# Kernel tuning notes

Measured on AMD Instinct MI355X. Metric: run time of the kernel, lower is better.

The kernel has to match this reference:

```python
import jax, jax.numpy as jnp
import numpy as np

N_NODES = 100000
N_EDGES = 1600000
IN_FEATS = 128
HEADS = 4
OUT_FEATS = 16
NEG_SLOPE = 0.2  # DGL GATConv default negative_slope


def setup_inputs() -> dict:
    key = jax.random.key(0)
    ks = jax.random.split(key, 7)
    feats = jax.random.normal(ks[0], (N_NODES, IN_FEATS), dtype=jnp.float32)
    W = jax.random.normal(ks[1], (HEADS * OUT_FEATS, IN_FEATS), dtype=jnp.float32) * 0.05
    attn_l = jax.random.normal(ks[2], (HEADS, OUT_FEATS), dtype=jnp.float32) * 0.1
    attn_r = jax.random.normal(ks[3], (HEADS, OUT_FEATS), dtype=jnp.float32) * 0.1
    bias = jax.random.normal(ks[4], (HEADS * OUT_FEATS,), dtype=jnp.float32) * 0.01
    src = jax.random.randint(ks[5], (N_EDGES,), 0, N_NODES, dtype=jnp.int64 if jax.config.jax_enable_x64 else jnp.int32)
    dst = jax.random.randint(ks[6], (N_EDGES,), 0, N_NODES, dtype=jnp.int64 if jax.config.jax_enable_x64 else jnp.int32)
    return {"feats": feats, "W": W, "attn_l": attn_l, "attn_r": attn_r,
            "bias": bias, "src": src, "dst": dst}


def reference(feats, W, attn_l, attn_r, bias, src, dst):
    """GATConv forward on a homogeneous graph built from concatenated edge lists.

    feats: [N, in_feats]; W: [H*F, in_feats]; attn_l/attn_r: [H, F]; bias: [H*F]
    src/dst: [E] edge endpoint indices. Returns [N, H, F] (DGL GATConv output).
    """
    N = feats.shape[0]
    H, F = attn_l.shape
    # Linear projection, per-head split: z [N, H, F]
    z = (feats @ W.T).reshape(N, H, F)
    # Per-node attention logits: el/er [N, H]
    el = jnp.einsum('nhf,hf->nh', z, attn_l)
    er = jnp.einsum('nhf,hf->nh', z, attn_r)
    # Per-edge unnormalized attention: e [E, H]
    e = jax.nn.leaky_relu(el[src] + er[dst], negative_slope=NEG_SLOPE)
    # Edge softmax over incoming edges of each destination node
    m = jax.ops.segment_max(e, dst, num_segments=N)           # [N, H]
    m = jnp.where(jnp.isfinite(m), m, jnp.zeros_like(m))      # guard empty segments
    ex = jnp.exp(e - m[dst])                                  # [E, H]
    denom = jax.ops.segment_sum(ex, dst, num_segments=N)      # [N, H]
    alpha = ex / denom[dst]                                   # [E, H]
    # Weighted message aggregation: scatter-add z[src] * alpha into dst
    msg = z[src] * alpha[:, :, None]                          # [E, H, F]
    out = jax.ops.segment_sum(msg, dst, num_segments=N)       # [N, H, F]
    return out + bias.reshape(1, H, F)
```

## Files before the change

kernel.cpp:

```cpp
#include <hip/hip_runtime.h>

#define N_NODES 100000
#define N_EDGES 1600000
#define IN_F    128
#define HEADS   4
#define OUT_F   16
#define HF      64
#define NEG_SLOPE 0.2f

#define BUCK    112
#define NBUCK   893
#define BSTRIDE 2048

#define BSC_CHUNK 8192
#define NB_BSC4 196

#define NB_MFMA2 782
#define NB_FUSED4 978

typedef __attribute__((ext_vector_type(8))) short short8;
typedef __attribute__((ext_vector_type(4))) float f32x4;

__device__ __forceinline__ short f2bf(float f) {
    union { float f; unsigned u; } v; v.f = f;
    return (short)((v.u + 0x7FFFu + ((v.u >> 16) & 1u)) >> 16);
}

__global__ __launch_bounds__(256) void k_prep(const float* __restrict__ W,
                                              const float* __restrict__ attn_l,
                                              const float* __restrict__ attn_r,
                                              unsigned short* __restrict__ Wfrag,
                                              int* __restrict__ gcur) {
    const int g = blockIdx.x, t = threadIdx.x;
    if (g >= 20) {
        int i = (g - 20) * 256 + t;
        if (i < 1024) gcur[i] = 0;
        return;
    }
    const int ct = g >> 2, kf = g & 3;
    #pragma unroll
    for (int e = 0; e < 2; ++e) {
        int off = e * 256 + t;
        int j = off & 7, lane = off >> 3;
        int n = lane & 15, qq = lane >> 4;
        int k = kf * 32 + qq * 8 + j;
        float v;
        if (ct < 4) {
            v = W[(size_t)(ct * 16 + n) * IN_F + k];
        } else if (n < 8) {
            int hh = n & 3;
            const float* at = (n < 4) ? attn_l : attn_r;
            v = 0.f;
            #pragma unroll
            for (int f = 0; f < 16; ++f)
                v += W[(size_t)(hh * 16 + f) * IN_F + k] * at[hh * 16 + f];
        } else {
            v = 0.f;
        }
        Wfrag[(size_t)g * 512 + off] = (unsigned short)f2bf(v);
    }
}

__global__ __launch_bounds__(512) void k_fused(const float* __restrict__ feats,
                                               const unsigned short* __restrict__ Wfrag,
                                               unsigned short* __restrict__ zb,
                                               float* __restrict__ el,
                                               float* __restrict__ er,
                                               const int* __restrict__ src,
                                               const int* __restrict__ dst,
                                               int* __restrict__ gcur,
                                               unsigned* __restrict__ bin) {
    const int t = threadIdx.x;

    if (blockIdx.x < NB_BSC4) {
        __shared__ unsigned sortedL[BSC_CHUNK];
        __shared__ int hist[NBUCK];
        __shared__ int cur[NBUCK];

        const int bid = blockIdx.x;
        const int start = bid * BSC_CHUNK;
        int end = start + BSC_CHUNK;
        if (end > N_EDGES) end = N_EDGES;

        for (int i = t; i < NBUCK; i += 512) hist[i] = 0;
        __syncthreads();

        for (int i = start + t; i < end; i += 512)
            atomicAdd(&hist[(unsigned)dst[i] / BUCK], 1);
        __syncthreads();

        if (t < 64) {
            int base = t * 14;
            int loc[14]; int acc = 0;
            #pragma unroll
            for (int k = 0; k < 14; ++k) {
                int idx = base + k;
                int v = (idx < NBUCK) ? hist[idx] : 0;
                loc[k] = acc; acc += v;
            }
            int x = acc;
            #pragma unroll
            for (int o = 1; o < 64; o <<= 1) {
                int y = __shfl_up(x, o);
                if (t >= o) x += y;
            }
            int excl = x - acc;
            #pragma unroll
            for (int k = 0; k < 14; ++k) {
                int idx = base + k;
                if (idx < NBUCK) cur[idx] = excl + loc[k];
            }
        }
        __syncthreads();

        for (int i = start + t; i < end; i += 512) {
            unsigned d = (unsigned)dst[i];
            unsigned b = d / BUCK;
            unsigned dl = d - b * BUCK;
            int pos = atomicAdd(&cur[b], 1);
            sortedL[pos] = (unsigned)src[i] | (dl << 17);
        }
        __syncthreads();

        for (int b = t; b < NBUCK; b += 512) {
            int n = hist[b];
            if (!n) continue;
            int lo = cur[b] - n;
            int gb = atomicAdd(&gcur[b], n);
            unsigned* dp = bin + (size_t)b * BSTRIDE;
            for (int k2 = 0; k2 < n; ++k2) {
                int gpos = gb + k2;
                if (gpos < BSTRIDE) dp[gpos] = sortedL[lo + k2];
            }
        }
        return;
    }

    const int bid = (int)blockIdx.x - NB_BSC4;

    const int grp = t >> 6;
    const int l = t & 63;
    const int q = l >> 4, n = l & 15;

    short8 bfrag[5][4];
    #pragma unroll
    for (int ct = 0; ct < 5; ++ct)
        #pragma unroll
        for (int kf = 0; kf < 4; ++kf)
            bfrag[ct][kf] = *(const short8*)(Wfrag + (size_t)((ct * 4 + kf) * 64 + l) * 8);

    int anode = bid * 128 + grp * 16 + n;
    int aclamp = anode < N_NODES ? anode : 0;
    const float* arow = feats + (size_t)aclamp * IN_F + q * 8;

    f32x4 acc[5];
    #pragma unroll
    for (int ct = 0; ct < 5; ++ct) acc[ct] = (f32x4){0.f, 0.f, 0.f, 0.f};

    #pragma unroll
    for (int kf = 0; kf < 4; ++kf) {
        float4 x = *(const float4*)(arow + kf * 32);
        float4 y = *(const float4*)(arow + kf * 32 + 4);
        short8 a;
        a[0] = f2bf(x.x); a[1] = f2bf(x.y); a[2] = f2bf(x.z); a[3] = f2bf(x.w);
        a[4] = f2bf(y.x); a[5] = f2bf(y.y); a[6] = f2bf(y.z); a[7] = f2bf(y.w);
        #pragma unroll
        for (int ct = 0; ct < 5; ++ct)
            acc[ct] = __builtin_amdgcn_mfma_f32_16x16x32_bf16(a, bfrag[ct][kf], acc[ct], 0, 0, 0);
    }

    #pragma unroll
    for (int reg = 0; reg < 4; ++reg) {
        int onode = bid * 128 + grp * 16 + q * 4 + reg;
        if (onode >= N_NODES) continue;
        #pragma unroll
        for (int ct = 0; ct < 4; ++ct)
            zb[(size_t)onode * HF + ct * 16 + n] = (unsigned short)f2bf(acc[ct][reg]);
        float v4 = acc[4][reg];
        if (n < 4)       el[onode * HEADS + n] = v4;
        else if (n < 8)  er[onode * HEADS + (n - 4)] = v4;
    }
}

__global__ __launch_bounds__(512) void k3_sort(const unsigned* __restrict__ bin,
                                               const int* __restrict__ gcur,
                                               const float* __restrict__ el,
                                               const float* __restrict__ er,
                                               const unsigned short* __restrict__ zb,
                                               const float* __restrict__ bias,
                                               float* __restrict__ out) {
    __shared__ unsigned raw[BSTRIDE];
    __shared__ unsigned sorted[BSTRIDE];
    __shared__ int hist[BUCK];
    __shared__ int noff[BUCK + 1];
    __shared__ int cur[BUCK];
    __shared__ int s[128];
    __shared__ float er_s[BUCK * HEADS];

    const int t = threadIdx.x;
    const int B = blockIdx.x;
    const int nodebase = B * BUCK;
    const unsigned* mybin = bin + (size_t)B * BSTRIDE;
    int cnt = gcur[B];
    if (cnt > BSTRIDE) cnt = BSTRIDE;

    if (t < BUCK) hist[t] = 0;
    if (t < BUCK * HEADS) {
        int g = nodebase * HEADS + t;
        er_s[t] = (g < N_NODES * HEADS) ? er[g] : 0.f;
    }
    for (int i = t; i < cnt; i += 512) raw[i] = mybin[i];
    __syncthreads();

    for (int i = t; i < cnt; i += 512)
        atomicAdd(&hist[raw[i] >> 17], 1);
    __syncthreads();

    if (t < 128) s[t] = (t < BUCK) ? hist[t] : 0;
    __syncthreads();
    for (int o = 1; o < 128; o <<= 1) {
        int x = (t < 128 && t >= o) ? s[t - o] : 0;
        __syncthreads();
        if (t < 128) s[t] += x;
        __syncthreads();
    }
    if (t < BUCK) {
        int excl = s[t] - hist[t];
        noff[t] = excl;
        cur[t] = excl;
    }
    if (t == 0) noff[BUCK] = s[BUCK - 1];
    __syncthreads();

    for (int i = t; i < cnt; i += 512) {
        unsigned p = raw[i];
        int pos = atomicAdd(&cur[p >> 17], 1);
        sorted[pos] = p & 0x1FFFF;
    }
    __syncthreads();

    const int wave = t >> 6, lane = t & 63;
    const int j = lane >> 3;
    const int c = lane & 7;
    const int h = c >> 1;
    const int jj = j & 3;
    const int sel = j >> 2;

    for (int p = wave; p < BUCK / 2; p += 8) {
        const int nl = p * 2 + sel;
        const int node = nodebase + nl;
        const int nlo = noff[nl], nhi = noff[nl + 1];
        const float er_d = er_s[nl * HEADS + h];

        float4 A0 = make_float4(0.f, 0.f, 0.f, 0.f);
        float4 A1 = make_float4(0.f, 0.f, 0.f, 0.f);
        float den = 0.f;
        for (int i = nlo + jj; i < nhi; i += 4) {
            int sN = (int)sorted[i];
            float x = el[sN * HEADS + h] + er_d;
            x = x > 0.f ? x : NEG_SLOPE * x;
            float ex = __expf(x);
            den += ex;
            uint4 v = *(const uint4*)(zb + (size_t)sN * HF + c * 8);
            A0.x += ex * __uint_as_float(v.x << 16);
            A0.y += ex * __uint_as_float(v.x & 0xFFFF0000u);
            A0.z += ex * __uint_as_float(v.y << 16);
            A0.w += ex * __uint_as_float(v.y & 0xFFFF0000u);
            A1.x += ex * __uint_as_float(v.z << 16);
            A1.y += ex * __uint_as_float(v.z & 0xFFFF0000u);
            A1.z += ex * __uint_as_float(v.w << 16);
            A1.w += ex * __uint_as_float(v.w & 0xFFFF0000u);
        }
        #pragma unroll
        for (int m = 8; m <= 16; m <<= 1) {
            A0.x += __shfl_xor(A0.x, m); A0.y += __shfl_xor(A0.y, m);
            A0.z += __shfl_xor(A0.z, m); A0.w += __shfl_xor(A0.w, m);
            A1.x += __shfl_xor(A1.x, m); A1.y += __shfl_xor(A1.y, m);
            A1.z += __shfl_xor(A1.z, m); A1.w += __shfl_xor(A1.w, m);
            den  += __shfl_xor(den,  m);
        }
        if (jj == 0 && node < N_NODES) {
            float4 b0 = *(const float4*)(bias + c * 8);
            float4 b1 = *(const float4*)(bias + c * 8 + 4);
            if (den > 0.f) {
                float inv = 1.f / den;
                b0.x += A0.x * inv; b0.y += A0.y * inv;
                b0.z += A0.z * inv; b0.w += A0.w * inv;
                b1.x += A1.x * inv; b1.y += A1.y * inv;
                b1.z += A1.z * inv; b1.w += A1.w * inv;
            }
            *(float4*)(out + (size_t)node * HF + c * 8) = b0;
            *(float4*)(out + (size_t)node * HF + c * 8 + 4) = b1;
        }
    }
}

extern "C" void kernel_launch(void* const* d_in, const int* in_sizes, int n_in,
                              void* d_out, int out_size, void* d_ws, size_t ws_size,
                              hipStream_t stream) {
    const float* feats  = (const float*)d_in[0];
    const float* W      = (const float*)d_in[1];
    const float* attn_l = (const float*)d_in[2];
    const float* attn_r = (const float*)d_in[3];
    const float* bias   = (const float*)d_in[4];
    const int*   src    = (const int*)d_in[5];
    const int*   dst    = (const int*)d_in[6];
    float* out = (float*)d_out;

    char* ws = (char*)d_ws;
    unsigned short* zb = (unsigned short*)ws;  ws += (size_t)N_NODES * HF * 2;
    float* el    = (float*)ws;                 ws += N_NODES * HEADS * 4;
    float* er    = (float*)ws;                 ws += N_NODES * HEADS * 4;
    unsigned short* Wfrag = (unsigned short*)ws; ws += 20 * 64 * 8 * 2;
    int*   gcur  = (int*)ws;                   ws += 1024 * 4;
    unsigned* bin = (unsigned*)ws;             ws += (size_t)NBUCK * BSTRIDE * 4;

    k_prep  <<<24,         256,  0, stream>>>(W, attn_l, attn_r, Wfrag, gcur);
    k_fused <<<NB_FUSED4,  512,  0, stream>>>(feats, Wfrag, zb, el, er, src, dst, gcur, bin);
    k3_sort <<<NBUCK,      512,  0, stream>>>(bin, gcur, el, er, zb, bias, out);
}
```

Baseline: 170.5 us.

## Interleave edge-binning and projection blocks, halve bin chunk, cache dst in registers

The fused kernel now interleaves its block roles by block index modulo 3: one binning block for every two MFMA projection blocks. Previously all binning blocks came first. The binning chunk is halved to 4096 edges, so 391 smaller binning blocks spread across the GPU alongside the compute blocks. Each thread also keeps its bucket and local-offset values in registers, so dst is read and divided only once instead of twice. The aim is better load balance and overlap between the memory-bound scatter and the compute-bound projection. The cost is more global atomics on gcur and shorter per-bucket runs written to bin.

```diff
diff --git a/kernel.cpp b/kernel.cpp
--- a/kernel.cpp
+++ b/kernel.cpp
@@ -12,11 +12,11 @@
 #define NBUCK   893
 #define BSTRIDE 2048
 
-#define BSC_CHUNK 8192
-#define NB_BSC4 196
+#define BSC_CHUNK 4096
+#define NB_BSC5 391
 
 #define NB_MFMA2 782
-#define NB_FUSED4 978
+#define NB_FUSED5 1173
 
 typedef __attribute__((ext_vector_type(8))) short short8;
 typedef __attribute__((ext_vector_type(4))) float f32x4;
@@ -71,13 +71,15 @@
                                                int* __restrict__ gcur,
                                                unsigned* __restrict__ bin) {
     const int t = threadIdx.x;
-
-    if (blockIdx.x < NB_BSC4) {
+    const unsigned bx = blockIdx.x;
+    const unsigned q3 = bx / 3u, r3 = bx % 3u;
+
+    if (r3 == 0u) {
         __shared__ unsigned sortedL[BSC_CHUNK];
         __shared__ int hist[NBUCK];
         __shared__ int cur[NBUCK];
 
-        const int bid = blockIdx.x;
+        const int bid = (int)q3;
         const int start = bid * BSC_CHUNK;
         int end = start + BSC_CHUNK;
         if (end > N_EDGES) end = N_EDGES;
@@ -85,8 +87,17 @@
         for (int i = t; i < NBUCK; i += 512) hist[i] = 0;
         __syncthreads();
 
-        for (int i = start + t; i < end; i += 512)
-            atomicAdd(&hist[(unsigned)dst[i] / BUCK], 1);
+        unsigned myv[8];
+        #pragma unroll
+        for (int k = 0; k < 8; ++k) {
+            int i = start + t + k * 512;
+            if (i < end) {
+                unsigned d = (unsigned)dst[i];
+                unsigned b = d / BUCK;
+                myv[k] = (b << 7) | (d - b * BUCK);
+                atomicAdd(&hist[b], 1);
+            } else myv[k] = 0xFFFFFFFFu;
+        }
         __syncthreads();
 
         if (t < 64) {
@@ -113,12 +124,15 @@
         }
         __syncthreads();
 
-        for (int i = start + t; i < end; i += 512) {
-            unsigned d = (unsigned)dst[i];
-            unsigned b = d / BUCK;
-            unsigned dl = d - b * BUCK;
-            int pos = atomicAdd(&cur[b], 1);
-            sortedL[pos] = (unsigned)src[i] | (dl << 17);
+        #pragma unroll
+        for (int k = 0; k < 8; ++k) {
+            if (myv[k] != 0xFFFFFFFFu) {
+                int i = start + t + k * 512;
+                unsigned b = myv[k] >> 7;
+                unsigned dl = myv[k] & 127u;
+                int pos = atomicAdd(&cur[b], 1);
+                sortedL[pos] = (unsigned)src[i] | (dl << 17);
+            }
         }
         __syncthreads();
 
@@ -136,7 +150,7 @@
         return;
     }
 
-    const int bid = (int)blockIdx.x - NB_BSC4;
+    const int bid = (int)(q3 * 2u + (r3 - 1u));
 
     const int grp = t >> 6;
     const int l = t & 63;
@@ -316,6 +330,6 @@
     unsigned* bin = (unsigned*)ws;             ws += (size_t)NBUCK * BSTRIDE * 4;
 
     k_prep  <<<24,         256,  0, stream>>>(W, attn_l, attn_r, Wfrag, gcur);
-    k_fused <<<NB_FUSED4,  512,  0, stream>>>(feats, Wfrag, zb, el, er, src, dst, gcur, bin);
+    k_fused <<<NB_FUSED5,  512,  0, stream>>>(feats, Wfrag, zb, el, er, src, dst, gcur, bin);
     k3_sort <<<NBUCK,      512,  0, stream>>>(bin, gcur, el, er, zb, bias, out);
 }
```

Result: no change. 171.4 us (+0.5%).
